# Optimization experiments

Hardware: AMD Instinct MI355X
Metric: run time of the kernel (lower is better)

Reference implementation:

```python
import jax, jax.numpy as jnp
import numpy as np

MAX_DET = 1000  # max_detections
CNS, SIN_YAW, COS_YAW, VX = 0, 6, 7, 8


def _decode_box(box):
    # box: [B, K, 10] -> [B, K, 10] decoded (x,y,z,w,l,h,yaw,vx,vy,vz)
    x, y, z = box[..., 0], box[..., 1], box[..., 2]
    w = jnp.exp(box[..., 3])
    l = jnp.exp(box[..., 4])
    h = jnp.exp(box[..., 5])
    yaw = jnp.arctan2(box[..., SIN_YAW], box[..., COS_YAW])  # code_size 10 > COS_YAW
    vx = box[..., VX]
    vy = box[..., VX + 1]
    vz = jnp.zeros_like(x)  # code_size == 10, no vz channel
    return jnp.stack([x, y, z, w, l, h, yaw, vx, vy, vz], axis=-1)


def setup_inputs() -> dict:
    key = jax.random.key(0)
    k1, k2, k3 = jax.random.split(key, 3)
    B, Q, C = 8, 100000, 10
    return {
        'cls_scores': jax.random.normal(k1, (B, Q, C), dtype=jnp.float32),
        'box_preds': jax.random.normal(k2, (B, Q, 10), dtype=jnp.float32),
        'quality': jax.random.normal(k3, (B, Q, 2), dtype=jnp.float32),
    }


def reference(cls_scores, box_preds, quality):
    B, Q, C = cls_scores.shape
    K = min(MAX_DET, Q * C)
    scores = jax.nn.sigmoid(cls_scores)
    # flattened top-k over (Q*C)
    topk_scores, indices = jax.lax.top_k(scores.reshape(B, Q * C), K)
    cls_ids = indices % C
    query_indices = indices // C
    # quality re-rank: scores *= sigmoid(centerness), then sort descending
    centerness = jnp.take_along_axis(quality[..., CNS], query_indices, axis=1)
    cls_scores_origin = topk_scores
    reranked = topk_scores * jax.nn.sigmoid(centerness)
    sort_idx = jnp.argsort(-reranked, axis=1)
    final_scores = jnp.take_along_axis(reranked, sort_idx, axis=1)
    query_indices = jnp.take_along_axis(query_indices, sort_idx, axis=1)
    cls_ids = jnp.take_along_axis(cls_ids, sort_idx, axis=1)
    raw_scores = jnp.take_along_axis(cls_scores_origin, sort_idx, axis=1)
    # gather boxes per batch: [B, K, 10]
    box = jnp.take_along_axis(box_preds, query_indices[..., None], axis=1)
    boxes_3d = _decode_box(box)
    labels_3d = cls_ids.astype(jnp.int64)
    return boxes_3d, final_scores, labels_3d, raw_scores
```

## Files before the change

kernel.cpp:

```cpp
#include <hip/hip_runtime.h>
#include <stdint.h>
#include <math.h>


#define BATCHES 8
#define NQ 100000
#define NEL 1000000
#define NVEC 250000
#define TOPK 1000
#define NBINS 4096
#define CAP 2048
#define NBLK 64
#define NTHR 512
#define STAGE_CAP 512
#define SELBLK 8
#define SRTBLK 8

__device__ __forceinline__ unsigned f2key(float f) {
    unsigned b = __float_as_uint(f);
    return b ^ ((b & 0x80000000u) ? 0xFFFFFFFFu : 0x80000000u);
}
__device__ __forceinline__ float key2f(unsigned k) {
    unsigned b = (k & 0x80000000u) ? (k ^ 0x80000000u) : ~k;
    return __uint_as_float(b);
}

__global__ __launch_bounds__(NTHR) void hist_kernel(const float* __restrict__ cls,
                                                    unsigned* __restrict__ ghist) {
    __shared__ unsigned lh[NBINS];
    const int b = blockIdx.x / NBLK;
    const int blk = blockIdx.x % NBLK;
    for (int i = threadIdx.x; i < NBINS; i += NTHR) lh[i] = 0;
    __syncthreads();
    const float4* src = (const float4*)(cls + (size_t)b * NEL);
    for (int i = blk * NTHR + threadIdx.x; i < NVEC; i += NBLK * NTHR) {
        float4 v = src[i];
        atomicAdd(&lh[f2key(v.x) >> 20], 1u);
        atomicAdd(&lh[f2key(v.y) >> 20], 1u);
        atomicAdd(&lh[f2key(v.z) >> 20], 1u);
        atomicAdd(&lh[f2key(v.w) >> 20], 1u);
    }
    __syncthreads();
    unsigned* gh = ghist + (size_t)b * NBINS;
    for (int i = threadIdx.x; i < NBINS; i += NTHR) {
        unsigned v = lh[i];
        if (v) atomicAdd(&gh[i], v);
    }
}

__global__ __launch_bounds__(256) void thresh_kernel(const unsigned* __restrict__ ghist,
                                                     unsigned* __restrict__ tbin) {
    __shared__ unsigned sh[NBINS];
    __shared__ unsigned coarse[256];
    const int b = blockIdx.x;
    for (int i = threadIdx.x; i < NBINS; i += 256) sh[i] = ghist[(size_t)b * NBINS + i];
    __syncthreads();
    unsigned s = 0;
    const int base = threadIdx.x * 16;
#pragma unroll
    for (int j = 0; j < 16; ++j) s += sh[base + j];
    coarse[threadIdx.x] = s;
    __syncthreads();
    if (threadIdx.x == 0) {
        unsigned acc = 0;
        int tb = 0;
        for (int c = 255; c >= 0; --c) {
            if (acc + coarse[c] >= (unsigned)TOPK) {
                for (int bin = c * 16 + 15; bin >= c * 16; --bin) {
                    acc += sh[bin];
                    if (acc >= (unsigned)TOPK) { tb = bin; break; }
                }
                break;
            }
            acc += coarse[c];
        }
        tbin[b] = (unsigned)tb;
    }
}

__global__ __launch_bounds__(NTHR) void collect_kernel(const float* __restrict__ cls,
                                                       const unsigned* __restrict__ tbin,
                                                       unsigned* __restrict__ cnt,
                                                       unsigned long long* __restrict__ cand) {
    __shared__ unsigned long long stage[STAGE_CAP];
    __shared__ unsigned lcnt;
    __shared__ unsigned gbase;
    const int b = blockIdx.x / NBLK;
    const int blk = blockIdx.x % NBLK;
    if (threadIdx.x == 0) lcnt = 0;
    __syncthreads();
    const unsigned tb = tbin[b];
    const float4* src = (const float4*)(cls + (size_t)b * NEL);
    unsigned long long* cb = cand + (size_t)b * CAP;
    for (int i = blk * NTHR + threadIdx.x; i < NVEC; i += NBLK * NTHR) {
        float4 v = src[i];
        float xs[4] = {v.x, v.y, v.z, v.w};
#pragma unroll
        for (int j = 0; j < 4; ++j) {
            unsigned k = f2key(xs[j]);
            if ((k >> 20) >= tb) {
                unsigned idx = (unsigned)(i * 4 + j);
                unsigned long long pack = ((unsigned long long)k << 32) |
                                          (unsigned long long)(0xFFFFFFFFu - idx);
                unsigned p = atomicAdd(&lcnt, 1u);
                if (p < STAGE_CAP) {
                    stage[p] = pack;
                } else {
                    unsigned pos = atomicAdd(&cnt[b], 1u);
                    if (pos < CAP) cb[pos] = pack;
                }
            }
        }
    }
    __syncthreads();
    unsigned n = lcnt < STAGE_CAP ? lcnt : STAGE_CAP;
    if (threadIdx.x == 0) gbase = atomicAdd(&cnt[b], n);
    __syncthreads();
    for (unsigned t = threadIdx.x; t < n; t += NTHR) {
        unsigned pos = gbase + t;
        if (pos < CAP) cb[pos] = stage[t];
    }
}

__global__ __launch_bounds__(256) void select_kernel(const float* __restrict__ quality,
                                                     const unsigned long long* __restrict__ cand,
                                                     const unsigned* __restrict__ cnt,
                                                     unsigned long long* __restrict__ top_rr,
                                                     float* __restrict__ top_s) {
    __shared__ unsigned long long arr[CAP];
    const int b = blockIdx.x / SELBLK;
    const int bk = blockIdx.x % SELBLK;
    const int tid = threadIdx.x;
    int n = (int)cnt[b];
    if (n > CAP) n = CAP;
    for (int i = tid; i < CAP; i += 256)
        arr[i] = (i < n) ? cand[(size_t)b * CAP + i] : 0ull;
    __syncthreads();

    const int ci = bk * 256 + tid;
    if (bk * 256 >= n) return;
    if (ci < n) {
        const unsigned long long m = arr[ci];
        int r = 0, j = 0;
        for (; j + 16 <= n; j += 16) {
            unsigned long long v0 = arr[j+0],  v1 = arr[j+1],  v2 = arr[j+2],  v3 = arr[j+3];
            unsigned long long v4 = arr[j+4],  v5 = arr[j+5],  v6 = arr[j+6],  v7 = arr[j+7];
            unsigned long long v8 = arr[j+8],  v9 = arr[j+9],  vA = arr[j+10], vB = arr[j+11];
            unsigned long long vC = arr[j+12], vD = arr[j+13], vE = arr[j+14], vF = arr[j+15];
            r += (v0 > m) + (v1 > m) + (v2 > m) + (v3 > m)
               + (v4 > m) + (v5 > m) + (v6 > m) + (v7 > m)
               + (v8 > m) + (v9 > m) + (vA > m) + (vB > m)
               + (vC > m) + (vD > m) + (vE > m) + (vF > m);
        }
        for (; j < n; ++j) r += (arr[j] > m);

        if (r < TOPK) {
            unsigned key = (unsigned)(m >> 32);
            unsigned idx = 0xFFFFFFFFu - (unsigned)(m & 0xFFFFFFFFu);
            unsigned q = idx / 10u;
            float logit = key2f(key);
            float s = (float)(1.0 / (1.0 + exp(-(double)logit)));
            float ctr = quality[((size_t)b * NQ + q) * 2];
            float cs = (float)(1.0 / (1.0 + exp(-(double)ctr)));
            float rr = s * cs;
            top_rr[(size_t)b * 1024 + r] = ((unsigned long long)__float_as_uint(rr) << 32) |
                                           (unsigned long long)(0xFFFFFFFFu - idx);
            top_s[(size_t)b * 1024 + r] = s;
        }
    }
}

__global__ __launch_bounds__(128) void sortdecode_kernel(const float* __restrict__ box_preds,
                                                         const unsigned long long* __restrict__ top_rr,
                                                         const float* __restrict__ top_s,
                                                         float* __restrict__ out) {
    __shared__ unsigned long long rr2[TOPK];
    const int b = blockIdx.x / SRTBLK;
    const int bk = blockIdx.x % SRTBLK;
    const int tid = threadIdx.x;
    for (int i = tid; i < TOPK; i += 128)
        rr2[i] = top_rr[(size_t)b * 1024 + i];
    __syncthreads();

    const int p = bk * 125 + tid;
    if (p < TOPK && tid < 125) {
        const unsigned long long mine = rr2[p];
        int r = 0, j = 0;
        for (; j + 16 <= TOPK; j += 16) {
            unsigned long long v0 = rr2[j+0],  v1 = rr2[j+1],  v2 = rr2[j+2],  v3 = rr2[j+3];
            unsigned long long v4 = rr2[j+4],  v5 = rr2[j+5],  v6 = rr2[j+6],  v7 = rr2[j+7];
            unsigned long long v8 = rr2[j+8],  v9 = rr2[j+9],  vA = rr2[j+10], vB = rr2[j+11];
            unsigned long long vC = rr2[j+12], vD = rr2[j+13], vE = rr2[j+14], vF = rr2[j+15];
            r += (v0 > mine) + (v1 > mine) + (v2 > mine) + (v3 > mine)
               + (v4 > mine) + (v5 > mine) + (v6 > mine) + (v7 > mine)
               + (v8 > mine) + (v9 > mine) + (vA > mine) + (vB > mine)
               + (vC > mine) + (vD > mine) + (vE > mine) + (vF > mine);
        }
        for (; j < TOPK; ++j) r += (rr2[j] > mine);

        unsigned idx = 0xFFFFFFFFu - (unsigned)(mine & 0xFFFFFFFFu);
        float rr = __uint_as_float((unsigned)(mine >> 32));
        unsigned q = idx / 10u;
        unsigned c = idx - q * 10u;
        float s = top_s[(size_t)b * 1024 + p];

        const size_t row = (size_t)b * TOPK + (size_t)r;
        out[(size_t)BATCHES * TOPK * 10 + row] = rr;
        out[(size_t)BATCHES * TOPK * 11 + row] = (float)c;
        out[(size_t)BATCHES * TOPK * 12 + row] = s;
        const float* bp = box_preds + ((size_t)b * NQ + q) * 10;
        float* ob = out + row * 10;
        ob[0] = bp[0];
        ob[1] = bp[1];
        ob[2] = bp[2];
        ob[3] = expf(bp[3]);
        ob[4] = expf(bp[4]);
        ob[5] = expf(bp[5]);
        ob[6] = atan2f(bp[6], bp[7]);
        ob[7] = bp[8];
        ob[8] = bp[9];
        ob[9] = 0.0f;
    }
}

extern "C" void kernel_launch(void* const* d_in, const int* in_sizes, int n_in,
                              void* d_out, int out_size, void* d_ws, size_t ws_size,
                              hipStream_t stream) {
    (void)in_sizes; (void)n_in; (void)out_size; (void)ws_size;
    const float* cls = (const float*)d_in[0];
    const float* box = (const float*)d_in[1];
    const float* qual = (const float*)d_in[2];
    float* out = (float*)d_out;
    char* ws = (char*)d_ws;
    unsigned* ghist = (unsigned*)ws;
    unsigned* cnt = (unsigned*)(ws + 131072);
    unsigned* tbin = (unsigned*)(ws + 131072 + 32);
    unsigned long long* cand = (unsigned long long*)(ws + 131072 + 64);
    unsigned long long* top_rr = (unsigned long long*)(ws + 131072 + 64 + 131072);
    float* top_s = (float*)(ws + 131072 + 64 + 131072 + 65536);

    hipMemsetAsync(d_ws, 0, 131072 + 32, stream);
    hist_kernel<<<BATCHES * NBLK, NTHR, 0, stream>>>(cls, ghist);
    thresh_kernel<<<BATCHES, 256, 0, stream>>>(ghist, tbin);
    collect_kernel<<<BATCHES * NBLK, NTHR, 0, stream>>>(cls, tbin, cnt, cand);
    select_kernel<<<BATCHES * SELBLK, 256, 0, stream>>>(qual, cand, cnt, top_rr, top_s);
    sortdecode_kernel<<<BATCHES * SRTBLK, 128, 0, stream>>>(box, top_rr, top_s, out);
}
```

Measured before the change: 147.8 us.

## Fuse histogram with speculative candidate collection to skip second input pass

The histogram pass now also collects every element above a fixed speculative bin into a spill buffer. The threshold kernel compacts from that buffer, so the second full read of the scores is skipped unless a flag shows the guess was wrong, in which case a repair kernel reruns the full collection. Per-block histograms are written out and reduced in the threshold kernel instead of using global atomics. Block and thread counts for select and sort are also retuned. The cost is extra shared-memory atomics in the first pass, plus a fixed speculative bin that suits this input distribution and only falls back to the slow path when it fails.

```diff
diff --git a/kernel.cpp b/kernel.cpp
--- a/kernel.cpp
+++ b/kernel.cpp
@@ -10,11 +10,13 @@
 #define TOPK 1000
 #define NBINS 4096
 #define CAP 2048
-#define NBLK 64
-#define NTHR 512
+#define NBLK_H 32
 #define STAGE_CAP 512
-#define SELBLK 8
-#define SRTBLK 8
+#define SPEC_CAP 8192
+#define SPEC_BIN 3075u
+#define SELBLK 16
+#define SELTHR 128
+#define SRTBLK 16
 
 __device__ __forceinline__ unsigned f2key(float f) {
     unsigned b = __float_as_uint(f);
@@ -25,43 +27,83 @@
     return __uint_as_float(b);
 }
 
-__global__ __launch_bounds__(NTHR) void hist_kernel(const float* __restrict__ cls,
-                                                    unsigned* __restrict__ ghist) {
+__global__ __launch_bounds__(512) void histspec_kernel(const float* __restrict__ cls,
+                                                       unsigned* __restrict__ phist,
+                                                       unsigned* __restrict__ speccnt,
+                                                       unsigned long long* __restrict__ spec) {
     __shared__ unsigned lh[NBINS];
-    const int b = blockIdx.x / NBLK;
-    const int blk = blockIdx.x % NBLK;
-    for (int i = threadIdx.x; i < NBINS; i += NTHR) lh[i] = 0;
+    __shared__ unsigned long long stg[STAGE_CAP];
+    __shared__ unsigned lcnt, gbase;
+    const int b = blockIdx.x / NBLK_H;
+    const int blk = blockIdx.x % NBLK_H;
+    for (int i = threadIdx.x; i < NBINS; i += 512) lh[i] = 0;
+    if (threadIdx.x == 0) lcnt = 0;
     __syncthreads();
     const float4* src = (const float4*)(cls + (size_t)b * NEL);
-    for (int i = blk * NTHR + threadIdx.x; i < NVEC; i += NBLK * NTHR) {
+    unsigned long long* sb = spec + (size_t)b * SPEC_CAP;
+    for (int i = blk * 512 + threadIdx.x; i < NVEC; i += NBLK_H * 512) {
         float4 v = src[i];
-        atomicAdd(&lh[f2key(v.x) >> 20], 1u);
-        atomicAdd(&lh[f2key(v.y) >> 20], 1u);
-        atomicAdd(&lh[f2key(v.z) >> 20], 1u);
-        atomicAdd(&lh[f2key(v.w) >> 20], 1u);
-    }
-    __syncthreads();
-    unsigned* gh = ghist + (size_t)b * NBINS;
-    for (int i = threadIdx.x; i < NBINS; i += NTHR) {
-        unsigned v = lh[i];
-        if (v) atomicAdd(&gh[i], v);
-    }
-}
-
-__global__ __launch_bounds__(256) void thresh_kernel(const unsigned* __restrict__ ghist,
-                                                     unsigned* __restrict__ tbin) {
+        float xs[4] = {v.x, v.y, v.z, v.w};
+#pragma unroll
+        for (int j = 0; j < 4; ++j) {
+            unsigned k = f2key(xs[j]);
+            atomicAdd(&lh[k >> 20], 1u);
+            if ((k >> 20) >= SPEC_BIN) {
+                unsigned long long pack = ((unsigned long long)k << 32) |
+                                          (unsigned long long)(0xFFFFFFFFu - (unsigned)(i * 4 + j));
+                unsigned p = atomicAdd(&lcnt, 1u);
+                if (p < STAGE_CAP) stg[p] = pack;
+                else {
+                    unsigned pos = atomicAdd(&speccnt[b], 1u);
+                    if (pos < SPEC_CAP) sb[pos] = pack;
+                }
+            }
+        }
+    }
+    __syncthreads();
+    uint4* ph = (uint4*)(phist + ((size_t)b * NBLK_H + blk) * NBINS);
+    for (int i = threadIdx.x; i < NBINS / 4; i += 512) ph[i] = ((uint4*)lh)[i];
+    unsigned n = lcnt < STAGE_CAP ? lcnt : STAGE_CAP;
+    if (threadIdx.x == 0) gbase = atomicAdd(&speccnt[b], n);
+    __syncthreads();
+    for (unsigned t = threadIdx.x; t < n; t += 512) {
+        unsigned pos = gbase + t;
+        if (pos < SPEC_CAP) sb[pos] = stg[t];
+    }
+}
+
+__global__ __launch_bounds__(256) void threshcompact_kernel(const unsigned* __restrict__ phist,
+                                                            const unsigned* __restrict__ speccnt,
+                                                            const unsigned long long* __restrict__ spec,
+                                                            unsigned* __restrict__ tbin,
+                                                            unsigned* __restrict__ cnt,
+                                                            unsigned long long* __restrict__ cand,
+                                                            unsigned* __restrict__ flag) {
     __shared__ unsigned sh[NBINS];
     __shared__ unsigned coarse[256];
+    __shared__ unsigned stb, lcnt;
     const int b = blockIdx.x;
-    for (int i = threadIdx.x; i < NBINS; i += 256) sh[i] = ghist[(size_t)b * NBINS + i];
-    __syncthreads();
-    unsigned s = 0;
-    const int base = threadIdx.x * 16;
-#pragma unroll
-    for (int j = 0; j < 16; ++j) s += sh[base + j];
-    coarse[threadIdx.x] = s;
-    __syncthreads();
-    if (threadIdx.x == 0) {
+    const int tid = threadIdx.x;
+    unsigned sum[16];
+#pragma unroll
+    for (int j = 0; j < 16; ++j) sum[j] = 0;
+    const unsigned* ph = phist + (size_t)b * NBLK_H * NBINS;
+    for (int h = 0; h < NBLK_H; ++h) {
+        const uint4* p4 = (const uint4*)(ph + h * NBINS + tid * 16);
+#pragma unroll
+        for (int g = 0; g < 4; ++g) {
+            uint4 v = p4[g];
+            sum[g * 4 + 0] += v.x; sum[g * 4 + 1] += v.y;
+            sum[g * 4 + 2] += v.z; sum[g * 4 + 3] += v.w;
+        }
+    }
+    unsigned csum = 0;
+#pragma unroll
+    for (int j = 0; j < 16; ++j) { sh[tid * 16 + j] = sum[j]; csum += sum[j]; }
+    coarse[tid] = csum;
+    if (tid == 0) lcnt = 0;
+    __syncthreads();
+    if (tid == 0) {
         unsigned acc = 0;
         int tb = 0;
         for (int c = 255; c >= 0; --c) {
@@ -75,38 +117,53 @@
             acc += coarse[c];
         }
         tbin[b] = (unsigned)tb;
-    }
-}
-
-__global__ __launch_bounds__(NTHR) void collect_kernel(const float* __restrict__ cls,
-                                                       const unsigned* __restrict__ tbin,
-                                                       unsigned* __restrict__ cnt,
-                                                       unsigned long long* __restrict__ cand) {
-    __shared__ unsigned long long stage[STAGE_CAP];
-    __shared__ unsigned lcnt;
-    __shared__ unsigned gbase;
-    const int b = blockIdx.x / NBLK;
-    const int blk = blockIdx.x % NBLK;
+        stb = (unsigned)tb;
+        if ((unsigned)tb < SPEC_BIN || speccnt[b] > SPEC_CAP) atomicOr(flag, 1u);
+    }
+    __syncthreads();
+    const unsigned tb = stb;
+    unsigned ns = speccnt[b]; if (ns > SPEC_CAP) ns = SPEC_CAP;
+    const unsigned long long* sb = spec + (size_t)b * SPEC_CAP;
+    unsigned long long* cb = cand + (size_t)b * CAP;
+    for (unsigned i = tid; i < ns; i += 256) {
+        unsigned long long v = sb[i];
+        if ((unsigned)(v >> 52) >= tb) {
+            unsigned p = atomicAdd(&lcnt, 1u);
+            if (p < CAP) cb[p] = v;
+        }
+    }
+    __syncthreads();
+    if (tid == 0) cnt[b] = lcnt < CAP ? lcnt : CAP;
+}
+
+__global__ __launch_bounds__(512) void repair_kernel(const float* __restrict__ cls,
+                                                     const unsigned* __restrict__ tbin,
+                                                     const unsigned* __restrict__ flag,
+                                                     unsigned* __restrict__ cntR,
+                                                     unsigned long long* __restrict__ candR) {
+    if (*flag == 0u) return;
+    __shared__ unsigned long long stg[STAGE_CAP];
+    __shared__ unsigned lcnt, gbase;
+    const int b = blockIdx.x / NBLK_H;
+    const int blk = blockIdx.x % NBLK_H;
     if (threadIdx.x == 0) lcnt = 0;
     __syncthreads();
     const unsigned tb = tbin[b];
     const float4* src = (const float4*)(cls + (size_t)b * NEL);
-    unsigned long long* cb = cand + (size_t)b * CAP;
-    for (int i = blk * NTHR + threadIdx.x; i < NVEC; i += NBLK * NTHR) {
+    unsigned long long* cb = candR + (size_t)b * CAP;
+    for (int i = blk * 512 + threadIdx.x; i < NVEC; i += NBLK_H * 512) {
         float4 v = src[i];
         float xs[4] = {v.x, v.y, v.z, v.w};
 #pragma unroll
         for (int j = 0; j < 4; ++j) {
             unsigned k = f2key(xs[j]);
             if ((k >> 20) >= tb) {
-                unsigned idx = (unsigned)(i * 4 + j);
                 unsigned long long pack = ((unsigned long long)k << 32) |
-                                          (unsigned long long)(0xFFFFFFFFu - idx);
+                                          (unsigned long long)(0xFFFFFFFFu - (unsigned)(i * 4 + j));
                 unsigned p = atomicAdd(&lcnt, 1u);
-                if (p < STAGE_CAP) {
-                    stage[p] = pack;
-                } else {
-                    unsigned pos = atomicAdd(&cnt[b], 1u);
+                if (p < STAGE_CAP) stg[p] = pack;
+                else {
+                    unsigned pos = atomicAdd(&cntR[b], 1u);
                     if (pos < CAP) cb[pos] = pack;
                 }
             }
@@ -114,31 +171,35 @@
     }
     __syncthreads();
     unsigned n = lcnt < STAGE_CAP ? lcnt : STAGE_CAP;
-    if (threadIdx.x == 0) gbase = atomicAdd(&cnt[b], n);
-    __syncthreads();
-    for (unsigned t = threadIdx.x; t < n; t += NTHR) {
+    if (threadIdx.x == 0) gbase = atomicAdd(&cntR[b], n);
+    __syncthreads();
+    for (unsigned t = threadIdx.x; t < n; t += 512) {
         unsigned pos = gbase + t;
-        if (pos < CAP) cb[pos] = stage[t];
-    }
-}
-
-__global__ __launch_bounds__(256) void select_kernel(const float* __restrict__ quality,
-                                                     const unsigned long long* __restrict__ cand,
-                                                     const unsigned* __restrict__ cnt,
-                                                     unsigned long long* __restrict__ top_rr,
-                                                     float* __restrict__ top_s) {
+        if (pos < CAP) cb[pos] = stg[t];
+    }
+}
+
+__global__ __launch_bounds__(SELTHR) void select_kernel(const float* __restrict__ quality,
+                                                        const unsigned long long* __restrict__ cand,
+                                                        const unsigned* __restrict__ cnt,
+                                                        const unsigned long long* __restrict__ candR,
+                                                        const unsigned* __restrict__ cntR,
+                                                        const unsigned* __restrict__ flag,
+                                                        unsigned long long* __restrict__ top_rr,
+                                                        float* __restrict__ top_s) {
     __shared__ unsigned long long arr[CAP];
     const int b = blockIdx.x / SELBLK;
     const int bk = blockIdx.x % SELBLK;
     const int tid = threadIdx.x;
-    int n = (int)cnt[b];
+    const bool rep = (*flag != 0u);
+    int n = (int)(rep ? cntR[b] : cnt[b]);
     if (n > CAP) n = CAP;
-    for (int i = tid; i < CAP; i += 256)
-        arr[i] = (i < n) ? cand[(size_t)b * CAP + i] : 0ull;
-    __syncthreads();
-
-    const int ci = bk * 256 + tid;
-    if (bk * 256 >= n) return;
+    if (bk * SELTHR >= n) return;
+    const unsigned long long* src = (rep ? candR : cand) + (size_t)b * CAP;
+    for (int i = tid; i < n; i += SELTHR) arr[i] = src[i];
+    __syncthreads();
+
+    const int ci = bk * SELTHR + tid;
     if (ci < n) {
         const unsigned long long m = arr[ci];
         int r = 0, j = 0;
@@ -170,20 +231,20 @@
     }
 }
 
-__global__ __launch_bounds__(128) void sortdecode_kernel(const float* __restrict__ box_preds,
-                                                         const unsigned long long* __restrict__ top_rr,
-                                                         const float* __restrict__ top_s,
-                                                         float* __restrict__ out) {
+__global__ __launch_bounds__(64) void sortdecode_kernel(const float* __restrict__ box_preds,
+                                                        const unsigned long long* __restrict__ top_rr,
+                                                        const float* __restrict__ top_s,
+                                                        float* __restrict__ out) {
     __shared__ unsigned long long rr2[TOPK];
     const int b = blockIdx.x / SRTBLK;
     const int bk = blockIdx.x % SRTBLK;
     const int tid = threadIdx.x;
-    for (int i = tid; i < TOPK; i += 128)
+    for (int i = tid; i < TOPK; i += 64)
         rr2[i] = top_rr[(size_t)b * 1024 + i];
     __syncthreads();
 
-    const int p = bk * 125 + tid;
-    if (p < TOPK && tid < 125) {
+    const int p = bk * 64 + tid;
+    if (p < TOPK) {
         const unsigned long long mine = rr2[p];
         int r = 0, j = 0;
         for (; j + 16 <= TOPK; j += 16) {
@@ -232,17 +293,22 @@
     const float* qual = (const float*)d_in[2];
     float* out = (float*)d_out;
     char* ws = (char*)d_ws;
-    unsigned* ghist = (unsigned*)ws;
-    unsigned* cnt = (unsigned*)(ws + 131072);
-    unsigned* tbin = (unsigned*)(ws + 131072 + 32);
-    unsigned long long* cand = (unsigned long long*)(ws + 131072 + 64);
-    unsigned long long* top_rr = (unsigned long long*)(ws + 131072 + 64 + 131072);
-    float* top_s = (float*)(ws + 131072 + 64 + 131072 + 65536);
-
-    hipMemsetAsync(d_ws, 0, 131072 + 32, stream);
-    hist_kernel<<<BATCHES * NBLK, NTHR, 0, stream>>>(cls, ghist);
-    thresh_kernel<<<BATCHES, 256, 0, stream>>>(ghist, tbin);
-    collect_kernel<<<BATCHES * NBLK, NTHR, 0, stream>>>(cls, tbin, cnt, cand);
-    select_kernel<<<BATCHES * SELBLK, 256, 0, stream>>>(qual, cand, cnt, top_rr, top_s);
-    sortdecode_kernel<<<BATCHES * SRTBLK, 128, 0, stream>>>(box, top_rr, top_s, out);
-}
+    unsigned* cnt = (unsigned*)ws;
+    unsigned* speccnt = (unsigned*)(ws + 32);
+    unsigned* tbin = (unsigned*)(ws + 64);
+    unsigned* cntR = (unsigned*)(ws + 96);
+    unsigned* flag = (unsigned*)(ws + 128);
+    unsigned long long* cand = (unsigned long long*)(ws + 256);
+    unsigned long long* candR = (unsigned long long*)(ws + 131328);
+    unsigned long long* top_rr = (unsigned long long*)(ws + 262400);
+    float* top_s = (float*)(ws + 327936);
+    unsigned long long* spec = (unsigned long long*)(ws + 360704);
+    unsigned* phist = (unsigned*)(ws + 884992);
+
+    hipMemsetAsync(d_ws, 0, 256, stream);
+    histspec_kernel<<<BATCHES * NBLK_H, 512, 0, stream>>>(cls, phist, speccnt, spec);
+    threshcompact_kernel<<<BATCHES, 256, 0, stream>>>(phist, speccnt, spec, tbin, cnt, cand, flag);
+    repair_kernel<<<BATCHES * NBLK_H, 512, 0, stream>>>(cls, tbin, flag, cntR, candR);
+    select_kernel<<<BATCHES * SELBLK, SELTHR, 0, stream>>>(qual, cand, cnt, candR, cntR, flag, top_rr, top_s);
+    sortdecode_kernel<<<BATCHES * SRTBLK, 64, 0, stream>>>(box, top_rr, top_s, out);
+}
```

Result: slower. 160.7 us (+8.8%).
